# Optimization experiments

Hardware: AMD Instinct MI355X
Metric: run time of the kernel (lower is better)

The kernel has to match this reference:

```python
import jax, jax.numpy as jnp
import numpy as np
import math

B, R, S, CE, H, C = 1, 384, 2048, 64, 8, 8
INF = 1e9
EPS = 1e-10


def setup_inputs() -> dict:
    key = jax.random.key(0)
    ks = jax.random.split(key, 10)
    m = jax.random.normal(ks[0], (B, R, S, CE), jnp.float32)
    mask = (jax.random.uniform(ks[1], (B, R, S)) > 0.1).astype(jnp.float32)
    glorot = lambda k, shp: (jax.random.normal(k, shp, jnp.float32)
                             * math.sqrt(2.0 / (shp[0] + shp[1])))
    Wq = glorot(ks[2], (H * C, CE))
    Wk = glorot(ks[3], (C, CE))
    Wv = glorot(ks[4], (C, CE))
    Wg = glorot(ks[5], (H * C, CE))
    bg = jnp.zeros((H * C,), jnp.float32)
    Wo = glorot(ks[6], (CE, H * C))
    bo = jnp.zeros((CE,), jnp.float32)
    add_to = jax.random.normal(ks[7], (B, S, R, CE), jnp.float32)
    return {"m": m, "mask": mask, "Wq": Wq, "Wk": Wk, "Wv": Wv,
            "Wg": Wg, "bg": bg, "Wo": Wo, "bo": bo, "add_to": add_to}


def reference(m, mask, Wq, Wk, Wv, Wg, bg, Wo, bo, add_to):
    # masked mean-pooled query over the extra-seq axis: [b, R, CE]
    q_num = jnp.sum(m * mask[..., None], axis=-2)
    q_den = jnp.sum(mask, axis=-1) + EPS
    q = q_num / q_den[..., None]
    # project + scale + split heads: [b, R, H, C]
    q = (q @ Wq.T) * math.sqrt(1.0 / C)
    q = q.reshape(q.shape[:-1] + (H, C))
    k = m @ Wk.T  # [b, R, S, C]
    v = m @ Wv.T  # [b, R, S, C]
    # attention logits [b, R, H, S] with mask bias then softmax over S
    a = jnp.einsum("brhc,brsc->brhs", q, k)
    bias = ((mask - 1.0) * INF)[..., None, :]  # [b, R, 1, S]
    a = jax.nn.softmax(a + bias, axis=-1)
    o = jnp.einsum("brhs,brsc->brhc", a, v)  # [b, R, H, C]
    # sigmoid gate per position: [b, R, S, H, C]
    g = jax.nn.sigmoid(m @ Wg.T + bg)
    g = g.reshape(g.shape[:-1] + (H, C))
    o = o[..., None, :, :] * g  # broadcast over S
    o = o.reshape(o.shape[:-2] + (H * C,))  # [b, R, S, H*C]
    # output projection, transpose (R<->S), fused residual add
    out = add_to + jnp.swapaxes(o @ Wo.T + bo, -2, -3)  # [b, S, R, CE]
    return out
```

## Files before the change

kernel.cpp:

```cpp
#include <hip/hip_runtime.h>

#define SS 2048
#define RR 384
#define CED 64

typedef __attribute__((ext_vector_type(8))) short bf16x8;
typedef __attribute__((ext_vector_type(4))) float f32x4;

__device__ __forceinline__ short f2bf(float f) {
  union { float f; unsigned u; } v; v.f = f;
  unsigned u = v.u;
  u += 0x7fffu + ((u >> 16) & 1u);
  return (short)(u >> 16);
}
__device__ __forceinline__ float bf2f(short s) {
  union { unsigned u; float f; } v;
  v.u = ((unsigned)(unsigned short)s) << 16;
  return v.f;
}

__global__ __launch_bounds__(256) void kW(const float* __restrict__ Wk,
                                          const float* __restrict__ Wv,
                                          const float* __restrict__ Wg,
                                          const float* __restrict__ Wo,
                                          short* __restrict__ wkv,
                                          short* __restrict__ wgb,
                                          short* __restrict__ wob) {
  int t = blockIdx.x * 256 + threadIdx.x;
  if (t < 1024) {
    int c16 = t >> 6, ce = t & 63;
    float v = (c16 < 8) ? Wk[c16 * 64 + ce] : Wv[(c16 - 8) * 64 + ce];
    wkv[t] = f2bf(v);
  }
  if (t < 4096) {
    wgb[t] = f2bf(Wg[t]);
    wob[t] = f2bf(Wo[t]);
  }
}

__global__ __launch_bounds__(256) void kA(const float* __restrict__ m,
                                          const float* __restrict__ mask,
                                          const float* __restrict__ Wq,
                                          const short* __restrict__ wkv,
                                          float* __restrict__ o_ws) {
  __shared__ __align__(16) short kv[SS][16];
  __shared__ __align__(16) float qs[64];
  __shared__ __align__(16) float qpart[4][64];
  __shared__ float redmax[4][8];
  __shared__ float redsum[4][8];
  __shared__ float ored[4][64];
  __shared__ float qden_l[4];

  const int r = blockIdx.x;
  const int tid = threadIdx.x;
  const int wave = tid >> 6, lane = tid & 63;
  const int l15 = lane & 15, quad = lane >> 4;

  bf16x8 bkv0 = *(const bf16x8*)(wkv + l15 * 64 + quad * 8);
  bf16x8 bkv1 = *(const bf16x8*)(wkv + l15 * 64 + 32 + quad * 8);

  float qdp = 0.f;
  float pp[16];
#pragma unroll
  for (int i = 0; i < 16; i++) pp[i] = 0.f;

  for (int s0 = wave * 16; s0 < SS; s0 += 64) {
    const int row = s0 + l15;
    const float* mrow = m + ((size_t)r * SS + row) * CED;
    f32x4 a0 = *(const f32x4*)(mrow + quad * 8);
    f32x4 a1 = *(const f32x4*)(mrow + quad * 8 + 4);
    f32x4 a2 = *(const f32x4*)(mrow + 32 + quad * 8);
    f32x4 a3 = *(const f32x4*)(mrow + 32 + quad * 8 + 4);
    float mk = mask[r * SS + row];
    qdp += mk;

    pp[0] += a0.x * mk;  pp[1] += a0.y * mk;  pp[2] += a0.z * mk;  pp[3] += a0.w * mk;
    pp[4] += a1.x * mk;  pp[5] += a1.y * mk;  pp[6] += a1.z * mk;  pp[7] += a1.w * mk;
    pp[8] += a2.x * mk;  pp[9] += a2.y * mk;  pp[10] += a2.z * mk; pp[11] += a2.w * mk;
    pp[12] += a3.x * mk; pp[13] += a3.y * mk; pp[14] += a3.z * mk; pp[15] += a3.w * mk;

    bf16x8 af0 = {f2bf(a0.x), f2bf(a0.y), f2bf(a0.z), f2bf(a0.w),
                  f2bf(a1.x), f2bf(a1.y), f2bf(a1.z), f2bf(a1.w)};
    bf16x8 af1 = {f2bf(a2.x), f2bf(a2.y), f2bf(a2.z), f2bf(a2.w),
                  f2bf(a3.x), f2bf(a3.y), f2bf(a3.z), f2bf(a3.w)};
    f32x4 acc = {0.f, 0.f, 0.f, 0.f};
    acc = __builtin_amdgcn_mfma_f32_16x16x32_bf16(af0, bkv0, acc, 0, 0, 0);
    acc = __builtin_amdgcn_mfma_f32_16x16x32_bf16(af1, bkv1, acc, 0, 0, 0);
#pragma unroll
    for (int rg = 0; rg < 4; rg++)
      kv[s0 + quad * 4 + rg][l15] = f2bf(acc[rg]);
  }

#pragma unroll
  for (int d = 1; d < 16; d <<= 1) {
#pragma unroll
    for (int i = 0; i < 16; i++) pp[i] += __shfl_xor(pp[i], d);
  }
#pragma unroll
  for (int d = 1; d < 16; d <<= 1) qdp += __shfl_xor(qdp, d);
  if (l15 == 0) {
#pragma unroll
    for (int i = 0; i < 8; i++) {
      qpart[wave][quad * 8 + i] = pp[i];
      qpart[wave][32 + quad * 8 + i] = pp[8 + i];
    }
  }
  if (lane == 0) qden_l[wave] = qdp;
  __syncthreads();

  if (wave == 0) {
    float qden = qden_l[0] + qden_l[1] + qden_l[2] + qden_l[3] + 1e-10f;
    float inv = 1.f / qden;
    const float* wqrow = Wq + lane * CED;
    float acc = 0.f;
    for (int ce = 0; ce < CED; ce++) {
      float qv = qpart[0][ce] + qpart[1][ce] + qpart[2][ce] + qpart[3][ce];
      acc += qv * wqrow[ce];
    }
    qs[lane] = acc * inv * 0.35355339059327373f;
  }
  __syncthreads();

  float q[64];
#pragma unroll
  for (int i = 0; i < 16; i++) ((f32x4*)q)[i] = ((const f32x4*)qs)[i];

  float lg[8][8];
  float mx[8];
#pragma unroll
  for (int h = 0; h < 8; h++) mx[h] = -3.0e38f;

#pragma unroll
  for (int j = 0; j < 8; j++) {
    int s = tid + 256 * j;
    bf16x8 k8 = *(const bf16x8*)&kv[s][0];
    float kf[8];
#pragma unroll
    for (int c = 0; c < 8; c++) kf[c] = bf2f(k8[c]);
    float bias = (mask[r * SS + s] - 1.f) * 1e9f;
#pragma unroll
    for (int h = 0; h < 8; h++) {
      float a = bias;
#pragma unroll
      for (int c = 0; c < 8; c++) a += q[h * 8 + c] * kf[c];
      lg[j][h] = a;
      mx[h] = fmaxf(mx[h], a);
    }
  }
#pragma unroll
  for (int d = 1; d < 64; d <<= 1) {
#pragma unroll
    for (int h = 0; h < 8; h++) mx[h] = fmaxf(mx[h], __shfl_xor(mx[h], d));
  }
  if (lane == 0) {
#pragma unroll
    for (int h = 0; h < 8; h++) redmax[wave][h] = mx[h];
  }
  __syncthreads();
  float Mh[8];
#pragma unroll
  for (int h = 0; h < 8; h++)
    Mh[h] = fmaxf(fmaxf(redmax[0][h], redmax[1][h]),
                  fmaxf(redmax[2][h], redmax[3][h]));

  float sm[8] = {0, 0, 0, 0, 0, 0, 0, 0};
#pragma unroll
  for (int j = 0; j < 8; j++) {
    int s = tid + 256 * j;
#pragma unroll
    for (int h = 0; h < 8; h++) {
      float p = __expf(lg[j][h] - Mh[h]);
      sm[h] += p;
      kv[s][h] = f2bf(p);
    }
  }
#pragma unroll
  for (int d = 1; d < 64; d <<= 1) {
#pragma unroll
    for (int h = 0; h < 8; h++) sm[h] += __shfl_xor(sm[h], d);
  }
  if (lane == 0) {
#pragma unroll
    for (int h = 0; h < 8; h++) redsum[wave][h] = sm[h];
  }
  __syncthreads();

  {
    int h = (tid >> 3) & 7, c = tid & 7, q4 = tid >> 6;
    float a0 = 0, a1 = 0, a2 = 0, a3 = 0;
    int sbeg = q4 * 512;
    for (int s = sbeg; s < sbeg + 512; s += 4) {
      a0 += bf2f(kv[s][h]) * bf2f(kv[s][8 + c]);
      a1 += bf2f(kv[s + 1][h]) * bf2f(kv[s + 1][8 + c]);
      a2 += bf2f(kv[s + 2][h]) * bf2f(kv[s + 2][8 + c]);
      a3 += bf2f(kv[s + 3][h]) * bf2f(kv[s + 3][8 + c]);
    }
    ored[q4][tid & 63] = (a0 + a1) + (a2 + a3);
  }
  __syncthreads();
  if (tid < 64) {
    int h = tid >> 3;
    float ssum = redsum[0][h] + redsum[1][h] + redsum[2][h] + redsum[3][h];
    float o = ored[0][tid] + ored[1][tid] + ored[2][tid] + ored[3][tid];
    o_ws[r * 64 + tid] = o / ssum;
  }
}

__global__ __launch_bounds__(256) void kB(const float* __restrict__ m,
                                          const float* __restrict__ add_to,
                                          const float* __restrict__ bg,
                                          const float* __restrict__ bo,
                                          const float* __restrict__ o_ws,
                                          const short* __restrict__ wg,
                                          const short* __restrict__ wo,
                                          float* __restrict__ out) {
  __shared__ __align__(16) short Tl[64][72];
  __shared__ __align__(16) float Yl[64][68];

  const int s = blockIdx.x;
  const int tid = threadIdx.x;
  const int wave = tid >> 6, lane = tid & 63;
  const int l15 = lane & 15, quad = lane >> 4;
  const int sp = tid >> 2, cb = (tid & 3) * 16;

  bf16x8 wgf[4][2], wof[4][2];
#pragma unroll
  for (int nt = 0; nt < 4; nt++) {
#pragma unroll
    for (int kc = 0; kc < 2; kc++) {
      wgf[nt][kc] = *(const bf16x8*)(wg + (nt * 16 + l15) * 64 + kc * 32 + quad * 8);
      wof[nt][kc] = *(const bf16x8*)(wo + (nt * 16 + l15) * 64 + kc * 32 + quad * 8);
    }
  }
  float bgv[4];
#pragma unroll
  for (int nt = 0; nt < 4; nt++) bgv[nt] = bg[nt * 16 + l15];
  f32x4 bov[4];
#pragma unroll
  for (int i = 0; i < 4; i++) bov[i] = *(const f32x4*)(bo + cb + i * 4);

  f32x4 mc[4];
  {
    const float* mp = m + ((size_t)(wave * 16 + l15) * SS + s) * CED;
    mc[0] = *(const f32x4*)(mp + quad * 8);
    mc[1] = *(const f32x4*)(mp + quad * 8 + 4);
    mc[2] = *(const f32x4*)(mp + 32 + quad * 8);
    mc[3] = *(const f32x4*)(mp + 32 + quad * 8 + 4);
  }

#pragma unroll
  for (int rt = 0; rt < 6; rt++) {
    const int r0 = rt * 64;

    f32x4 mn[4];
    if (rt < 5) {
      const float* mp = m + ((size_t)(r0 + 64 + wave * 16 + l15) * SS + s) * CED;
      mn[0] = *(const f32x4*)(mp + quad * 8);
      mn[1] = *(const f32x4*)(mp + quad * 8 + 4);
      mn[2] = *(const f32x4*)(mp + 32 + quad * 8);
      mn[3] = *(const f32x4*)(mp + 32 + quad * 8 + 4);
    }

    const float* ap = add_to + ((size_t)s * RR + r0 + sp) * CED + cb;
    f32x4 at0 = ((const f32x4*)ap)[0];
    f32x4 at1 = ((const f32x4*)ap)[1];
    f32x4 at2 = ((const f32x4*)ap)[2];
    f32x4 at3 = ((const f32x4*)ap)[3];

    float o16[4][4];
    {
      const float* ob = o_ws + (r0 + wave * 16 + quad * 4) * 64 + l15;
#pragma unroll
      for (int rg = 0; rg < 4; rg++)
#pragma unroll
        for (int nt = 0; nt < 4; nt++)
          o16[rg][nt] = ob[rg * 64 + nt * 16];
    }

    f32x4 acc[4] = {{0,0,0,0},{0,0,0,0},{0,0,0,0},{0,0,0,0}};
    {
      bf16x8 af0 = {f2bf(mc[0].x), f2bf(mc[0].y), f2bf(mc[0].z), f2bf(mc[0].w),
                    f2bf(mc[1].x), f2bf(mc[1].y), f2bf(mc[1].z), f2bf(mc[1].w)};
      bf16x8 af1 = {f2bf(mc[2].x), f2bf(mc[2].y), f2bf(mc[2].z), f2bf(mc[2].w),
                    f2bf(mc[3].x), f2bf(mc[3].y), f2bf(mc[3].z), f2bf(mc[3].w)};
#pragma unroll
      for (int nt = 0; nt < 4; nt++) {
        acc[nt] = __builtin_amdgcn_mfma_f32_16x16x32_bf16(af0, wgf[nt][0], acc[nt], 0, 0, 0);
        acc[nt] = __builtin_amdgcn_mfma_f32_16x16x32_bf16(af1, wgf[nt][1], acc[nt], 0, 0, 0);
      }
    }
#pragma unroll
    for (int nt = 0; nt < 4; nt++) {
#pragma unroll
      for (int rg = 0; rg < 4; rg++) {
        float val = acc[nt][rg] + bgv[nt];
        float gt = 1.f / (1.f + __expf(-val));
        Tl[wave * 16 + quad * 4 + rg][nt * 16 + l15] = f2bf(gt * o16[rg][nt]);
      }
    }
    __syncthreads();

    f32x4 acc2[4] = {{0,0,0,0},{0,0,0,0},{0,0,0,0},{0,0,0,0}};
#pragma unroll
    for (int kc = 0; kc < 2; kc++) {
      bf16x8 af = *(const bf16x8*)&Tl[wave * 16 + l15][kc * 32 + quad * 8];
#pragma unroll
      for (int nt = 0; nt < 4; nt++)
        acc2[nt] = __builtin_amdgcn_mfma_f32_16x16x32_bf16(af, wof[nt][kc], acc2[nt], 0, 0, 0);
    }
#pragma unroll
    for (int nt = 0; nt < 4; nt++) {
#pragma unroll
      for (int rg = 0; rg < 4; rg++)
        Yl[wave * 16 + quad * 4 + rg][nt * 16 + l15] = acc2[nt][rg];
    }
    __syncthreads();

    float* op = out + ((size_t)s * RR + r0 + sp) * CED + cb;
    f32x4 y0 = *(const f32x4*)&Yl[sp][cb];
    f32x4 y1 = *(const f32x4*)&Yl[sp][cb + 4];
    f32x4 y2 = *(const f32x4*)&Yl[sp][cb + 8];
    f32x4 y3 = *(const f32x4*)&Yl[sp][cb + 12];
    ((f32x4*)op)[0] = at0 + y0 + bov[0];
    ((f32x4*)op)[1] = at1 + y1 + bov[1];
    ((f32x4*)op)[2] = at2 + y2 + bov[2];
    ((f32x4*)op)[3] = at3 + y3 + bov[3];

    if (rt < 5) {
      mc[0] = mn[0]; mc[1] = mn[1]; mc[2] = mn[2]; mc[3] = mn[3];
    }
  }
}

extern "C" void kernel_launch(void* const* d_in, const int* in_sizes, int n_in,
                              void* d_out, int out_size, void* d_ws, size_t ws_size,
                              hipStream_t stream) {
  const float* m      = (const float*)d_in[0];
  const float* mask   = (const float*)d_in[1];
  const float* Wq     = (const float*)d_in[2];
  const float* Wk     = (const float*)d_in[3];
  const float* Wv     = (const float*)d_in[4];
  const float* Wg     = (const float*)d_in[5];
  const float* bg     = (const float*)d_in[6];
  const float* Wo     = (const float*)d_in[7];
  const float* bo     = (const float*)d_in[8];
  const float* add_to = (const float*)d_in[9];
  float* out = (float*)d_out;

  char* ws = (char*)d_ws;
  float* o_ws = (float*)ws;
  short* wkv  = (short*)(ws + 98304);
  short* wgb  = (short*)(ws + 98304 + 2048);
  short* wob  = (short*)(ws + 98304 + 2048 + 8192);

  hipLaunchKernelGGL(kW, dim3(16),   dim3(256), 0, stream, Wk, Wv, Wg, Wo, wkv, wgb, wob);
  hipLaunchKernelGGL(kA, dim3(384),  dim3(256), 0, stream, m, mask, Wq, wkv, o_ws);
  hipLaunchKernelGGL(kB, dim3(2048), dim3(256), 0, stream, m, add_to, bg, bo, o_ws, wgb, wob, out);
}
```

Baseline: 554.2 us.

## Split kB across two blocks per column and drop block barriers via per-wave LDS

The gate/output-projection kernel now launches two blocks per s position, each covering half of the R rows, which doubles the grid. Each wave now writes and reads only its own 16-row slice of the shared staging buffers, with the epilogue remapped so lanes store rows owned by the same wave. That removes both __syncthreads per row tile and lets waves progress independently, aimed at better latency hiding in this memory-bound kernel. In exchange the weight fragments and biases are loaded twice as often, and each block has a shorter prefetch pipeline.

```diff
diff --git a/kernel.cpp b/kernel.cpp
--- a/kernel.cpp
+++ b/kernel.cpp
@@ -214,14 +214,16 @@
                                           const short* __restrict__ wg,
                                           const short* __restrict__ wo,
                                           float* __restrict__ out) {
-  __shared__ __align__(16) short Tl[64][72];
-  __shared__ __align__(16) float Yl[64][68];
-
-  const int s = blockIdx.x;
+  __shared__ __align__(16) short Tl[4][16][72];
+  __shared__ __align__(16) float Yl[4][16][68];
+
+  const int bx = blockIdx.x;
+  const int s = bx >> 1;
+  const int half = bx & 1;
   const int tid = threadIdx.x;
   const int wave = tid >> 6, lane = tid & 63;
   const int l15 = lane & 15, quad = lane >> 4;
-  const int sp = tid >> 2, cb = (tid & 3) * 16;
+  const int spw = lane >> 2, cb = (lane & 3) * 16;
 
   bf16x8 wgf[4][2], wof[4][2];
 #pragma unroll
@@ -239,9 +241,11 @@
 #pragma unroll
   for (int i = 0; i < 4; i++) bov[i] = *(const f32x4*)(bo + cb + i * 4);
 
+  const int rbase = half * 192;
+
   f32x4 mc[4];
   {
-    const float* mp = m + ((size_t)(wave * 16 + l15) * SS + s) * CED;
+    const float* mp = m + ((size_t)(rbase + wave * 16 + l15) * SS + s) * CED;
     mc[0] = *(const f32x4*)(mp + quad * 8);
     mc[1] = *(const f32x4*)(mp + quad * 8 + 4);
     mc[2] = *(const f32x4*)(mp + 32 + quad * 8);
@@ -249,11 +253,11 @@
   }
 
 #pragma unroll
-  for (int rt = 0; rt < 6; rt++) {
-    const int r0 = rt * 64;
+  for (int rtl = 0; rtl < 3; rtl++) {
+    const int r0 = rbase + rtl * 64;
 
     f32x4 mn[4];
-    if (rt < 5) {
+    if (rtl < 2) {
       const float* mp = m + ((size_t)(r0 + 64 + wave * 16 + l15) * SS + s) * CED;
       mn[0] = *(const f32x4*)(mp + quad * 8);
       mn[1] = *(const f32x4*)(mp + quad * 8 + 4);
@@ -261,7 +265,7 @@
       mn[3] = *(const f32x4*)(mp + 32 + quad * 8 + 4);
     }
 
-    const float* ap = add_to + ((size_t)s * RR + r0 + sp) * CED + cb;
+    const float* ap = add_to + ((size_t)s * RR + r0 + wave * 16 + spw) * CED + cb;
     f32x4 at0 = ((const f32x4*)ap)[0];
     f32x4 at1 = ((const f32x4*)ap)[1];
     f32x4 at2 = ((const f32x4*)ap)[2];
@@ -295,15 +299,14 @@
       for (int rg = 0; rg < 4; rg++) {
         float val = acc[nt][rg] + bgv[nt];
         float gt = 1.f / (1.f + __expf(-val));
-        Tl[wave * 16 + quad * 4 + rg][nt * 16 + l15] = f2bf(gt * o16[rg][nt]);
+        Tl[wave][quad * 4 + rg][nt * 16 + l15] = f2bf(gt * o16[rg][nt]);
       }
     }
-    __syncthreads();
 
     f32x4 acc2[4] = {{0,0,0,0},{0,0,0,0},{0,0,0,0},{0,0,0,0}};
 #pragma unroll
     for (int kc = 0; kc < 2; kc++) {
-      bf16x8 af = *(const bf16x8*)&Tl[wave * 16 + l15][kc * 32 + quad * 8];
+      bf16x8 af = *(const bf16x8*)&Tl[wave][l15][kc * 32 + quad * 8];
 #pragma unroll
       for (int nt = 0; nt < 4; nt++)
         acc2[nt] = __builtin_amdgcn_mfma_f32_16x16x32_bf16(af, wof[nt][kc], acc2[nt], 0, 0, 0);
@@ -312,21 +315,20 @@
     for (int nt = 0; nt < 4; nt++) {
 #pragma unroll
       for (int rg = 0; rg < 4; rg++)
-        Yl[wave * 16 + quad * 4 + rg][nt * 16 + l15] = acc2[nt][rg];
-    }
-    __syncthreads();
-
-    float* op = out + ((size_t)s * RR + r0 + sp) * CED + cb;
-    f32x4 y0 = *(const f32x4*)&Yl[sp][cb];
-    f32x4 y1 = *(const f32x4*)&Yl[sp][cb + 4];
-    f32x4 y2 = *(const f32x4*)&Yl[sp][cb + 8];
-    f32x4 y3 = *(const f32x4*)&Yl[sp][cb + 12];
+        Yl[wave][quad * 4 + rg][nt * 16 + l15] = acc2[nt][rg];
+    }
+
+    float* op = out + ((size_t)s * RR + r0 + wave * 16 + spw) * CED + cb;
+    f32x4 y0 = *(const f32x4*)&Yl[wave][spw][cb];
+    f32x4 y1 = *(const f32x4*)&Yl[wave][spw][cb + 4];
+    f32x4 y2 = *(const f32x4*)&Yl[wave][spw][cb + 8];
+    f32x4 y3 = *(const f32x4*)&Yl[wave][spw][cb + 12];
     ((f32x4*)op)[0] = at0 + y0 + bov[0];
     ((f32x4*)op)[1] = at1 + y1 + bov[1];
     ((f32x4*)op)[2] = at2 + y2 + bov[2];
     ((f32x4*)op)[3] = at3 + y3 + bov[3];
 
-    if (rt < 5) {
+    if (rtl < 2) {
       mc[0] = mn[0]; mc[1] = mn[1]; mc[2] = mn[2]; mc[3] = mn[3];
     }
   }
@@ -355,5 +357,5 @@
 
   hipLaunchKernelGGL(kW, dim3(16),   dim3(256), 0, stream, Wk, Wv, Wg, Wo, wkv, wgb, wob);
   hipLaunchKernelGGL(kA, dim3(384),  dim3(256), 0, stream, m, mask, Wq, wkv, o_ws);
-  hipLaunchKernelGGL(kB, dim3(2048), dim3(256), 0, stream, m, add_to, bg, bo, o_ws, wgb, wob, out);
-}
+  hipLaunchKernelGGL(kB, dim3(4096), dim3(256), 0, stream, m, add_to, bg, bo, o_ws, wgb, wob, out);
+}
```

Measured after the change: 579.5 us. +4.6%, slower.
